# Kernel tuning notes

Measured on AMD Instinct MI355X. Metric: run time of the kernel, lower is better.

The kernel has to match this reference:

```python
import jax, jax.numpy as jnp
import numpy as np
from jax import lax

PRE_NMS_TOPN = 2000
POST_NMS_TOPN = 1000
NMS_THRESH = 0.7
MIN_BOX_SIZE = 4.0
BBOX_XFORM_CLIP = 4.135  # log(1000/16), standard clamp on dw/dh


def setup_inputs() -> dict:
    key = jax.random.key(0)
    k1, k2, k3, k4 = jax.random.split(key, 4)
    B, N = 8, 250000
    H, W = 800, 1333
    rpn_bbox_pred = jax.random.normal(k1, (B, N, 4), jnp.float32) * 0.5
    objectness = jax.random.normal(k2, (B, N), jnp.float32)
    # realistic anchors: centers inside image, sizes in [16, 256]
    ctr = jax.random.uniform(k3, (N, 2), jnp.float32) * jnp.array([W, H], jnp.float32)
    wh = jax.random.uniform(k4, (N, 2), jnp.float32) * 240.0 + 16.0
    anchors = jnp.concatenate([ctr - 0.5 * wh, ctr + 0.5 * wh], axis=-1)
    return {"rpn_bbox_pred": rpn_bbox_pred, "objectness": objectness,
            "anchors": anchors, "height": H, "width": W}


def _decode_clip(anchors, deltas, height, width):
    # anchors (1,N,4) broadcast against deltas (B,N,4); boxes are x1,y1,x2,y2
    aw = anchors[..., 2] - anchors[..., 0]
    ah = anchors[..., 3] - anchors[..., 1]
    ax = anchors[..., 0] + 0.5 * aw
    ay = anchors[..., 1] + 0.5 * ah
    dx, dy = deltas[..., 0], deltas[..., 1]
    dw = jnp.minimum(deltas[..., 2], BBOX_XFORM_CLIP)
    dh = jnp.minimum(deltas[..., 3], BBOX_XFORM_CLIP)
    px = dx * aw + ax
    py = dy * ah + ay
    pw = jnp.exp(dw) * aw
    ph = jnp.exp(dh) * ah
    x1 = jnp.clip(px - 0.5 * pw, 0.0, float(width))
    y1 = jnp.clip(py - 0.5 * ph, 0.0, float(height))
    x2 = jnp.clip(px + 0.5 * pw, 0.0, float(width))
    y2 = jnp.clip(py + 0.5 * ph, 0.0, float(height))
    return jnp.stack([x1, y1, x2, y2], axis=-1)


def _pairwise_iou(boxes):
    # boxes (K,4) -> iou (K,K)
    x1, y1, x2, y2 = boxes[:, 0], boxes[:, 1], boxes[:, 2], boxes[:, 3]
    area = (x2 - x1) * (y2 - y1)
    iw = jnp.maximum(jnp.minimum(x2[:, None], x2[None, :]) - jnp.maximum(x1[:, None], x1[None, :]), 0.0)
    ih = jnp.maximum(jnp.minimum(y2[:, None], y2[None, :]) - jnp.maximum(y1[:, None], y1[None, :]), 0.0)
    inter = iw * ih
    return inter / (area[:, None] + area[None, :] - inter + 1e-9)


def _nms_keep(boxes, valid):
    # sequential greedy NMS over score-sorted boxes (K,4); returns keep mask (K,)
    iou = lax.stop_gradient(_pairwise_iou(boxes))
    idxs = jnp.arange(PRE_NMS_TOPN)
    def body(i, keep):
        sup = (iou[i] > NMS_THRESH) & keep[i] & (idxs > i)
        return keep & (~sup)
    return lax.fori_loop(0, PRE_NMS_TOPN, body, valid)


def _per_image(boxes, scores):
    # boxes (N,4), scores (N,)
    ws = boxes[:, 2] - boxes[:, 0]
    hs = boxes[:, 3] - boxes[:, 1]
    size_ok = (ws >= MIN_BOX_SIZE) & (hs >= MIN_BOX_SIZE)
    masked = jnp.where(size_ok, scores, -jnp.inf)
    top_s, order = lax.top_k(masked, PRE_NMS_TOPN)   # descending sort + pre-NMS topN
    top_boxes = boxes[order]                          # (PRE,4)
    valid = top_s > -jnp.inf                          # boxes surviving size filter
    keep = _nms_keep(top_boxes, valid)
    # take first POST_NMS_TOPN kept boxes in score order (fixed-shape padding)
    sel = jnp.sort(jnp.where(keep, jnp.arange(PRE_NMS_TOPN), PRE_NMS_TOPN))[:POST_NMS_TOPN]
    out_valid = sel < PRE_NMS_TOPN
    sel_c = jnp.minimum(sel, PRE_NMS_TOPN - 1)
    out = jnp.where(out_valid[:, None], top_boxes[sel_c], 0.0)
    return out, out_valid


def reference(rpn_bbox_pred, objectness, anchors, height, width):
    proposals = _decode_clip(anchors[None], rpn_bbox_pred, height, width)  # (B,N,4)
    out, valid = jax.vmap(_per_image)(proposals, objectness)
    # padded equivalent of the ragged per-image list: (B,POST,4) boxes + (B,POST) validity
    return out, valid
```

## Files before the change

### kernel.cpp

```cpp
#include <hip/hip_runtime.h>
#include <hip/hip_bf16.h>

#define NBUCK 8192
#define P1B   32
#define CAP   4096
#define TOPN  2000
#define NP2   2048
#define OUTN  1000
#define NST   64
#define NSLOT 8
#define SLOTW 2048

typedef unsigned int u32x4 __attribute__((ext_vector_type(4)));
typedef __attribute__((address_space(1))) const unsigned GUP;
typedef __attribute__((address_space(3))) unsigned LUP;

__device__ __forceinline__ float4 decode_box(const float4 a, const float4 d, float W, float H) {
    float aw = a.z - a.x;
    float ah = a.w - a.y;
    float ax = a.x + 0.5f * aw;
    float ay = a.y + 0.5f * ah;
    float dw = fminf(d.z, 4.135f);
    float dh = fminf(d.w, 4.135f);
    float px = d.x * aw + ax;
    float py = d.y * ah + ay;
    float pw = expf(dw) * aw;
    float ph = expf(dh) * ah;
    float4 r;
    r.x = fminf(fmaxf(px - 0.5f * pw, 0.0f), W);
    r.y = fminf(fmaxf(py - 0.5f * ph, 0.0f), H);
    r.z = fminf(fmaxf(px + 0.5f * pw, 0.0f), W);
    r.w = fminf(fmaxf(py + 0.5f * ph, 0.0f), H);
    return r;
}

__device__ __forceinline__ unsigned score_key(const float4 a, const float4 d, float W, float H, float s) {
    float4 b = decode_box(a, d, W, H);
    bool ok = ((b.z - b.x) >= 4.0f) && ((b.w - b.y) >= 4.0f);
    float ms = ok ? s : -INFINITY;
    unsigned u = __float_as_uint(ms);
    return (u & 0x80000000u) ? ~u : (u | 0x80000000u);
}

__global__ void k_zero(u32x4* __restrict__ hist) {
    hist[blockIdx.x * 256 + threadIdx.x] = (u32x4){0u, 0u, 0u, 0u};
}

__global__ void __launch_bounds__(1024) k_pass1(const float* __restrict__ pred,
        const float* __restrict__ obj, const float* __restrict__ anch,
        const int* __restrict__ Hp, const int* __restrict__ Wp,
        unsigned* __restrict__ keys, unsigned* __restrict__ hist,
        unsigned* __restrict__ cnt, unsigned* __restrict__ remInit, int N) {
    __shared__ unsigned h[2 * NBUCK];
    int t = threadIdx.x;
    int b = blockIdx.y, g = blockIdx.x;
    if (g == 0 && t < 64) { if (t == 0) cnt[b * 64] = 0; remInit[b * 64 + t] = 0; }
    for (int i = t; i < 2 * NBUCK; i += 1024) h[i] = 0;
    __syncthreads();
    int chunk = (N + P1B - 1) / P1B;
    int base = g * chunk;
    int end = base + chunk; if (end > N) end = N;
    float W = (float)*Wp, H = (float)*Hp;
    unsigned cp = (t & 1) ? NBUCK : 0;
    for (int n = base + t; n < end; n += 1024) {
        float4 a = ((const float4*)anch)[n];
        float4 d = ((const float4*)pred)[(size_t)b * N + n];
        float s = obj[(size_t)b * N + n];
        unsigned key = score_key(a, d, W, H, s);
        keys[(size_t)b * N + n] = key;
        atomicAdd(&h[cp + (key >> 19)], 1u);
    }
    __syncthreads();
    for (int i = t; i < NBUCK; i += 1024) {
        unsigned v = h[i] + h[NBUCK + i];
        if (v) atomicAdd(&hist[b * NBUCK + i], v);
    }
}

__global__ void k_scan(const unsigned* __restrict__ hist, unsigned* __restrict__ Lb) {
    __shared__ unsigned h[NBUCK];
    __shared__ unsigned csum[256];
    __shared__ unsigned suf[256];
    __shared__ int tcS;
    __shared__ unsigned beforeS;
    int b = blockIdx.x, t = threadIdx.x;
    const unsigned* src = hist + (size_t)b * NBUCK;
    for (int i = t * 4; i < NBUCK; i += 1024) {
        uint4 v = *(const uint4*)(src + i);
        h[i] = v.x; h[i + 1] = v.y; h[i + 2] = v.z; h[i + 3] = v.w;
    }
    if (t == 0) tcS = -1;
    __syncthreads();
    unsigned s = 0;
    for (int j = 0; j < 32; j++) s += h[t * 32 + j];
    csum[t] = s; suf[t] = s;
    __syncthreads();
    for (int d = 1; d < 256; d <<= 1) {
        unsigned v = (t + d < 256) ? suf[t + d] : 0;
        __syncthreads();
        suf[t] += v;
        __syncthreads();
    }
    if (suf[t] >= (unsigned)TOPN && (t == 255 || suf[t + 1] < (unsigned)TOPN)) {
        tcS = t; beforeS = (t == 255) ? 0u : suf[t + 1];
    }
    __syncthreads();
    if (t == 0) {
        unsigned L = 0;
        int tc = tcS;
        if (tc >= 0) {
            unsigned r = beforeS;
            for (int bkt = tc * 32 + 31;; bkt--) {
                r += h[bkt];
                if (r >= (unsigned)TOPN || bkt == tc * 32) { L = (unsigned)bkt; break; }
            }
        }
        Lb[b] = L;
    }
}

__global__ void k_collect(const unsigned* __restrict__ keys, const unsigned* __restrict__ Lb,
                          unsigned* __restrict__ count, unsigned long long* __restrict__ cand,
                          int N) {
    __shared__ unsigned lk[1024], ln[1024];
    __shared__ unsigned lcnt, lbase;
    int b = blockIdx.y, t = threadIdx.x;
    if (t == 0) lcnt = 0;
    __syncthreads();
    unsigned L = Lb[b];
    const unsigned* kb = keys + (size_t)b * N;
    int e = blockIdx.x * 256 + t;
    int n0 = e * 4;
    if (n0 + 3 < N) {
        uint4 kv = ((const uint4*)kb)[e];
        if ((kv.x >> 19) >= L) { unsigned p = atomicAdd(&lcnt, 1u); lk[p] = kv.x; ln[p] = n0; }
        if ((kv.y >> 19) >= L) { unsigned p = atomicAdd(&lcnt, 1u); lk[p] = kv.y; ln[p] = n0 + 1; }
        if ((kv.z >> 19) >= L) { unsigned p = atomicAdd(&lcnt, 1u); lk[p] = kv.z; ln[p] = n0 + 2; }
        if ((kv.w >> 19) >= L) { unsigned p = atomicAdd(&lcnt, 1u); lk[p] = kv.w; ln[p] = n0 + 3; }
    } else {
        for (int j = 0; j < 4; j++) {
            int n = n0 + j;
            if (n < N) {
                unsigned k = kb[n];
                if ((k >> 19) >= L) { unsigned p = atomicAdd(&lcnt, 1u); lk[p] = k; ln[p] = n; }
            }
        }
    }
    __syncthreads();
    if (t == 0) lbase = atomicAdd(&count[b * 64], lcnt);
    __syncthreads();
    unsigned c = lcnt, bs = lbase;
    for (unsigned i = t; i < c; i += 256) {
        unsigned pos = bs + i;
        if (pos < CAP) cand[(size_t)b * CAP + pos] =
            ((unsigned long long)lk[i] << 32) | (unsigned)(~ln[i]);
    }
}

#define REGX(e, p, d, lo)  ((lo) == (d) ? ((e) >= (p) ? (e) : (p)) : ((e) >= (p) ? (p) : (e)))

__global__ void __launch_bounds__(256) k_sort1(unsigned long long* __restrict__ cand,
        const unsigned* __restrict__ count) {
    __shared__ unsigned long long s[512];
    int b = blockIdx.x >> 3, g = blockIdx.x & 7;
    int t = threadIdx.x;
    unsigned cnt = count[b * 64]; if (cnt > CAP) cnt = CAP;
    unsigned long long* cb = cand + (size_t)b * CAP + g * 512;
    if ((unsigned)(g * 512) >= cnt) {
        cb[t] = 0ULL; cb[t + 256] = 0ULL;
        return;
    }
    int g0 = g * 512 + t, g1 = g * 512 + t + 256;
    unsigned long long e0 = (g0 < (int)cnt) ? cb[t] : 0ULL;
    unsigned long long e1 = (g1 < (int)cnt) ? cb[t + 256] : 0ULL;

    #pragma unroll
    for (int k = 2; k <= 64; k <<= 1) {
        bool d0 = ((g0 & k) == 0);
        bool d1 = ((g1 & k) == 0);
        #pragma unroll
        for (int j = k >> 1; j >= 1; j >>= 1) {
            bool lo = ((t & j) == 0);
            unsigned long long p0 = __shfl_xor(e0, j, 64);
            unsigned long long p1 = __shfl_xor(e1, j, 64);
            e0 = REGX(e0, p0, d0, lo);
            e1 = REGX(e1, p1, d1, lo);
        }
    }
    for (int k = 128; k <= 512; k <<= 1) {
        s[t] = e0; s[t + 256] = e1;
        __syncthreads();
        for (int j = k >> 1; j >= 64; j >>= 1) {
            int i = ((t & ~(j - 1)) << 1) | (t & (j - 1));
            int l = i + j;
            bool desc = (((g * 512 + i) & k) == 0);
            unsigned long long x = s[i], y = s[l];
            if (desc ? (x < y) : (x > y)) { s[i] = y; s[l] = x; }
            __syncthreads();
        }
        e0 = s[t]; e1 = s[t + 256];
        bool d0 = ((g0 & k) == 0);
        bool d1 = ((g1 & k) == 0);
        #pragma unroll
        for (int j = 32; j >= 1; j >>= 1) {
            bool lo = ((t & j) == 0);
            unsigned long long p0 = __shfl_xor(e0, j, 64);
            unsigned long long p1 = __shfl_xor(e1, j, 64);
            e0 = REGX(e0, p0, d0, lo);
            e1 = REGX(e1, p1, d1, lo);
        }
    }
    cb[t] = e0; cb[t + 256] = e1;
}

__global__ void __launch_bounds__(1024) k_sort2(const unsigned long long* __restrict__ cand,
        const unsigned* __restrict__ count,
        const float* __restrict__ pred, const float* __restrict__ anch,
        const int* __restrict__ Hp, const int* __restrict__ Wp,
        float4* __restrict__ topbox, unsigned* __restrict__ remInit, int N) {
    __shared__ unsigned long long s[CAP];
    int b = blockIdx.x, t = threadIdx.x;
    const unsigned long long* cb = cand + (size_t)b * CAP;
    unsigned cnt = count[b * 64]; if (cnt > CAP) cnt = CAP;
    unsigned long long e0, e1;
    if (cnt <= 2048) {
        e0 = cb[t]; e1 = cb[t + 1024];
        for (int k = 1024; k <= 2048; k <<= 1) {
            s[t] = e0; s[t + 1024] = e1;
            __syncthreads();
            for (int j = k >> 1; j >= 64; j >>= 1) {
                int i = ((t & ~(j - 1)) << 1) | (t & (j - 1));
                int l = i + j;
                bool desc = ((i & k) == 0);
                unsigned long long x = s[i], y = s[l];
                if (desc ? (x < y) : (x > y)) { s[i] = y; s[l] = x; }
                __syncthreads();
            }
            e0 = s[t]; e1 = s[t + 1024];
            bool d0 = ((t & k) == 0);
            bool d1 = (((t + 1024) & k) == 0);
            #pragma unroll
            for (int j = 32; j >= 1; j >>= 1) {
                bool lo = ((t & j) == 0);
                unsigned long long p0 = __shfl_xor(e0, j, 64);
                unsigned long long p1 = __shfl_xor(e1, j, 64);
                e0 = REGX(e0, p0, d0, lo);
                e1 = REGX(e1, p1, d1, lo);
            }
        }
    } else {
        unsigned long long f0 = cb[t], f1 = cb[t + 1024], f2 = cb[t + 2048], f3 = cb[t + 3072];
        for (int k = 1024; k <= 4096; k <<= 1) {
            s[t] = f0; s[t + 1024] = f1; s[t + 2048] = f2; s[t + 3072] = f3;
            __syncthreads();
            for (int j = k >> 1; j >= 64; j >>= 1) {
                #pragma unroll
                for (int cc = 0; cc < 2; cc++) {
                    int c = t + cc * 1024;
                    int i = ((c & ~(j - 1)) << 1) | (c & (j - 1));
                    int l = i + j;
                    bool desc = ((i & k) == 0);
                    unsigned long long x = s[i], y = s[l];
                    if (desc ? (x < y) : (x > y)) { s[i] = y; s[l] = x; }
                }
                __syncthreads();
            }
            f0 = s[t]; f1 = s[t + 1024]; f2 = s[t + 2048]; f3 = s[t + 3072];
            bool d0 = ((t & k) == 0);
            bool d1 = (((t + 1024) & k) == 0);
            bool d2 = (((t + 2048) & k) == 0);
            bool d3 = (((t + 3072) & k) == 0);
            #pragma unroll
            for (int j = 32; j >= 1; j >>= 1) {
                bool lo = ((t & j) == 0);
                unsigned long long p0 = __shfl_xor(f0, j, 64);
                unsigned long long p1 = __shfl_xor(f1, j, 64);
                unsigned long long p2 = __shfl_xor(f2, j, 64);
                unsigned long long p3 = __shfl_xor(f3, j, 64);
                f0 = REGX(f0, p0, d0, lo);
                f1 = REGX(f1, p1, d1, lo);
                f2 = REGX(f2, p2, d2, lo);
                f3 = REGX(f3, p3, d3, lo);
            }
        }
        e0 = f0; e1 = f1;
    }
    float W = (float)*Wp, H = (float)*Hp;
    #pragma unroll
    for (int m = 0; m < 2; m++) {
        unsigned long long v = m ? e1 : e0;
        int r = t + m * 1024;
        unsigned key = (unsigned)(v >> 32);
        bool valid = key > 0x007FFFFFu;
        float4 outb = {0.f, 0.f, 0.f, 0.f};
        if (valid) {
            unsigned idx = ~((unsigned)v);
            float4 a = ((const float4*)anch)[idx];
            float4 d = ((const float4*)pred)[(size_t)b * N + idx];
            outb = decode_box(a, d, W, H);
        }
        topbox[(size_t)b * NP2 + r] = outb;
        if (r < TOPN && !valid) atomicOr(&remInit[b * 64 + (r >> 5)], 1u << (r & 31));
    }
}

__global__ void __launch_bounds__(256) k_mask(const float4* __restrict__ topbox,
                                              unsigned* __restrict__ maskT) {
    const double MID = 23488103.0 / 33554432.0;
    __shared__ float4 bx[NP2];
    __shared__ float ar[NP2];
    int b = blockIdx.y, cp = blockIdx.x;
    int t = threadIdx.x;
    int j0 = cp * 32;
    for (int i = j0 + t; i < NP2; i += 256) {
        float4 v = topbox[(size_t)b * NP2 + i];
        bx[i] = v;
        ar[i] = (v.z - v.x) * (v.w - v.y);
    }
    __syncthreads();
    int r = t & 31;
    int wg = t >> 5;
    #pragma unroll
    for (int half = 0; half < 2; half++) {
        int c = half ? (63 - cp) : cp;
        int i = c * 32 + r;
        float4 bi = bx[i];
        float areai = ar[i];
        unsigned* outc = maskT + ((size_t)(b * NST + c)) * SLOTW;
        for (int w = wg; w < c; w += 8) outc[w * 32 + r] = 0u;
        for (int w = c + wg; w < 64; w += 8) {
            unsigned bits = 0;
            int jbase = w * 32;
            #pragma unroll
            for (int jj = 0; jj < 32; jj++) {
                int j = jbase + jj;
                float4 bj = bx[j];
                float iw = fmaxf(fminf(bi.z, bj.z) - fmaxf(bi.x, bj.x), 0.0f);
                float ih = fmaxf(fminf(bi.w, bj.w) - fmaxf(bi.y, bj.y), 0.0f);
                float inter = iw * ih;
                float denom = areai + ar[j] - inter + 1e-9f;
                if ((double)inter >= MID * (double)denom) bits |= (1u << jj);
            }
            if (w == c) bits &= ~((2u << r) - 1u);
            outc[w * 32 + r] = bits;
        }
    }
}

__global__ void __launch_bounds__(512) k_nms(const unsigned* __restrict__ maskT,
        const unsigned* __restrict__ remInit, const float4* __restrict__ topbox,
        float* __restrict__ out, int B) {
    __shared__ __align__(16) unsigned smbuf[NSLOT * SLOTW];
    __shared__ int ready[NST];
    __shared__ int consumed;
    __shared__ int stop;
    int b = blockIdx.x;
    int t = threadIdx.x;
    const unsigned* m = maskT + (size_t)b * NST * SLOTW;

    float4* ob = (float4*)out + (size_t)b * OUTN;
    for (int i = t; i < OUTN; i += 512) ob[i] = make_float4(0.f, 0.f, 0.f, 0.f);
    float* vout = out + (size_t)B * (OUTN * 4) + (size_t)b * OUTN;
    for (int i = t; i < OUTN; i += 512) vout[i] = 0.0f;

    if (t < NST) ready[t] = 0;
    if (t == 0) { consumed = 0; stop = 0; }
    __syncthreads();

    unsigned removed = 0xFFFFFFFFu;

    if (t >= 64) {
        int w = t >> 6;
        int lam = t & 63;
        int base = ((lam >> 3) << 5) + ((((lam & 7) ^ ((lam >> 3) & 7))) << 2);
        #pragma unroll 1
        for (int s = w - 1; s < NST; s += 7) {
            if (__hip_atomic_load(&stop, __ATOMIC_RELAXED, __HIP_MEMORY_SCOPE_WORKGROUP)) break;
            while (__hip_atomic_load(&consumed, __ATOMIC_ACQUIRE,
                   __HIP_MEMORY_SCOPE_WORKGROUP) < s - (NSLOT - 1))
                __builtin_amdgcn_s_sleep(2);
            const unsigned* gs = m + (size_t)s * SLOTW + base;
            unsigned* sl = smbuf + (s & (NSLOT - 1)) * SLOTW;
            #pragma unroll
            for (int i = 0; i < 8; i++)
                __builtin_amdgcn_global_load_lds((GUP*)(gs + i * 256),
                                                 (LUP*)(sl + i * 256), 16, 0, 0);
            asm volatile("s_waitcnt vmcnt(0)" ::: "memory");
            if (lam == 0) __hip_atomic_store(&ready[s], 1, __ATOMIC_RELEASE,
                                             __HIP_MEMORY_SCOPE_WORKGROUP);
        }
    } else {
        removed = remInit[b * 64 + t];
        if (t == 62) removed |= 0xFFFF0000u;
        if (t == 63) removed = 0xFFFFFFFFu;
        int e = t & 7;
        int keptRun = 0;
        #pragma unroll 1
        for (int s = 0; s < NST; s++) {
            while (!__hip_atomic_load(&ready[s], __ATOMIC_ACQUIRE,
                   __HIP_MEMORY_SCOPE_WORKGROUP))
                __builtin_amdgcn_s_sleep(2);
            const u32x4* sq = (const u32x4*)(smbuf + (s & (NSLOT - 1)) * SLOTW) + t * 8;
            unsigned R[32];
            #pragma unroll
            for (int k = 0; k < 8; k++) *(u32x4*)&R[k << 2] = sq[k ^ e];
            __builtin_amdgcn_sched_group_barrier(0x100, 8, 0);
            unsigned alive = ~__builtin_amdgcn_readlane(removed, s);
            unsigned Is[32];
            #pragma unroll
            for (int q = 0; q < 32; q++) Is[q] = __builtin_amdgcn_readlane(R[q], s);
            #pragma unroll
            for (int q = 0; q < 32; q++) alive &= ~(((alive >> q) & 1u) ? Is[q] : 0u);
            unsigned a0 = 0, a1 = 0, a2 = 0, a3 = 0;
            #pragma unroll
            for (int q = 0; q < 32; q += 4) {
                a0 |= ((alive >> q) & 1u)       ? R[q]     : 0u;
                a1 |= ((alive >> (q + 1)) & 1u) ? R[q + 1] : 0u;
                a2 |= ((alive >> (q + 2)) & 1u) ? R[q + 2] : 0u;
                a3 |= ((alive >> (q + 3)) & 1u) ? R[q + 3] : 0u;
            }
            removed |= (a0 | a1) | (a2 | a3);
            keptRun += __popc(~__builtin_amdgcn_readlane(removed, s));
            if (keptRun >= OUTN) {
                if (t == 0) {
                    __hip_atomic_store(&stop, 1, __ATOMIC_RELAXED, __HIP_MEMORY_SCOPE_WORKGROUP);
                    __hip_atomic_store(&consumed, NST, __ATOMIC_RELEASE, __HIP_MEMORY_SCOPE_WORKGROUP);
                }
                break;
            }
            if (t == 0) __hip_atomic_store(&consumed, s + 1, __ATOMIC_RELEASE,
                                           __HIP_MEMORY_SCOPE_WORKGROUP);
        }
        unsigned keep = ~removed;
        int cnt = __popc(keep);
        int ex = cnt;
        for (int off = 1; off < 64; off <<= 1) {
            int v = __shfl_up(ex, off, 64);
            if (t >= off) ex += v;
        }
        ex -= cnt;
        int pos = ex;
        for (int j = 0; j < 32; j++) {
            if ((keep >> j) & 1u) {
                if (pos < OUTN) {
                    float4 bxv = topbox[(size_t)b * NP2 + t * 32 + j];
                    ob[pos] = bxv;
                    vout[pos] = 1.0f;
                }
                pos++;
            }
        }
    }
}

extern "C" void kernel_launch(void* const* d_in, const int* in_sizes, int n_in,
                              void* d_out, int out_size, void* d_ws, size_t ws_size,
                              hipStream_t stream) {
    const float* pred = (const float*)d_in[0];
    const float* obj  = (const float*)d_in[1];
    const float* anch = (const float*)d_in[2];
    const int* Hp = (const int*)d_in[3];
    const int* Wp = (const int*)d_in[4];
    int N = in_sizes[2] / 4;
    int B = in_sizes[1] / N;

    char* ws = (char*)d_ws;
    size_t off = 0;
    auto take = [&](size_t bytes) { void* p = ws + off; off = (off + bytes + 255) & ~(size_t)255; return p; };

    size_t regA_bytes = (size_t)B * N * 4;
    size_t mask_bytes = (size_t)B * NST * SLOTW * 4;
    char* regA = (char*)take(regA_bytes > mask_bytes ? regA_bytes : mask_bytes);
    unsigned* keys  = (unsigned*)regA;
    unsigned* maskT = (unsigned*)regA;
    unsigned* hist           = (unsigned*)take((size_t)B * NBUCK * 4);
    unsigned long long* cand = (unsigned long long*)take((size_t)B * CAP * 8);
    float4* topbox           = (float4*)take((size_t)B * NP2 * 16);
    unsigned* cnt            = (unsigned*)take((size_t)B * 64 * 4);
    unsigned* Lb             = (unsigned*)take((size_t)B * 64 * 4);
    unsigned* remInit        = (unsigned*)take((size_t)B * 64 * 4);

    k_zero   <<<(B * NBUCK) / 1024, 256, 0, stream>>>((u32x4*)hist);
    k_pass1  <<<dim3(P1B, B), 1024, 0, stream>>>(pred, obj, anch, Hp, Wp, keys, hist, cnt, remInit, N);
    k_scan   <<<B, 256, 0, stream>>>(hist, Lb);
    k_collect<<<dim3((N + 1023) / 1024, B), 256, 0, stream>>>(keys, Lb, cnt, cand, N);
    k_sort1  <<<B * 8, 256, 0, stream>>>(cand, cnt);
    k_sort2  <<<B, 1024, 0, stream>>>(cand, cnt, pred, anch, Hp, Wp, topbox, remInit, N);
    k_mask   <<<dim3(32, B), 256, 0, stream>>>(topbox, maskT);
    k_nms    <<<B, 512, 0, stream>>>(maskT, remInit, topbox, (float*)d_out, B);
}
```

Baseline: 118.2 us.

## Fuse histogram scan into pass1 via last-block election; coarsen collect blocks

After: 131.5 us. 11.2% more time.

```diff
diff --git a/kernel.cpp b/kernel.cpp
--- a/kernel.cpp
+++ b/kernel.cpp
@@ -42,16 +42,19 @@
     return (u & 0x80000000u) ? ~u : (u | 0x80000000u);
 }
 
-__global__ void k_zero(u32x4* __restrict__ hist) {
-    hist[blockIdx.x * 256 + threadIdx.x] = (u32x4){0u, 0u, 0u, 0u};
+__global__ void k_zero(unsigned* __restrict__ p, int nq) {
+    int i = blockIdx.x * 256 + threadIdx.x;
+    if (i < nq) ((u32x4*)p)[i] = (u32x4){0u, 0u, 0u, 0u};
 }
 
 __global__ void __launch_bounds__(1024) k_pass1(const float* __restrict__ pred,
         const float* __restrict__ obj, const float* __restrict__ anch,
         const int* __restrict__ Hp, const int* __restrict__ Wp,
         unsigned* __restrict__ keys, unsigned* __restrict__ hist,
+        unsigned* __restrict__ done, unsigned* __restrict__ Lb,
         unsigned* __restrict__ cnt, unsigned* __restrict__ remInit, int N) {
     __shared__ unsigned h[2 * NBUCK];
+    __shared__ int lastFlag;
     int t = threadIdx.x;
     int b = blockIdx.y, g = blockIdx.x;
     if (g == 0 && t < 64) { if (t == 0) cnt[b * 64] = 0; remInit[b * 64 + t] = 0; }
@@ -75,41 +78,45 @@
         unsigned v = h[i] + h[NBUCK + i];
         if (v) atomicAdd(&hist[b * NBUCK + i], v);
     }
-}
-
-__global__ void k_scan(const unsigned* __restrict__ hist, unsigned* __restrict__ Lb) {
-    __shared__ unsigned h[NBUCK];
-    __shared__ unsigned csum[256];
-    __shared__ unsigned suf[256];
-    __shared__ int tcS;
-    __shared__ unsigned beforeS;
-    int b = blockIdx.x, t = threadIdx.x;
-    const unsigned* src = hist + (size_t)b * NBUCK;
-    for (int i = t * 4; i < NBUCK; i += 1024) {
-        uint4 v = *(const uint4*)(src + i);
-        h[i] = v.x; h[i + 1] = v.y; h[i + 2] = v.z; h[i + 3] = v.w;
-    }
-    if (t == 0) tcS = -1;
-    __syncthreads();
-    unsigned s = 0;
-    for (int j = 0; j < 32; j++) s += h[t * 32 + j];
-    csum[t] = s; suf[t] = s;
+    if (t == 0) {
+        __threadfence();
+        unsigned dcnt = __hip_atomic_fetch_add(&done[b], 1u, __ATOMIC_ACQ_REL,
+                                               __HIP_MEMORY_SCOPE_AGENT);
+        lastFlag = (dcnt == P1B - 1);
+    }
+    __syncthreads();
+    if (!lastFlag) return;
+    __threadfence();
+    unsigned* csum = h + NBUCK;
+    unsigned* suf  = h + NBUCK + 256;
+    int*      tcS  = (int*)(h + NBUCK + 512);
+    unsigned* befS = h + NBUCK + 513;
+    for (int i = t; i < NBUCK; i += 1024)
+        h[i] = __hip_atomic_load(&hist[b * NBUCK + i], __ATOMIC_RELAXED,
+                                 __HIP_MEMORY_SCOPE_AGENT);
+    if (t == 0) *tcS = -1;
+    __syncthreads();
+    if (t < 256) {
+        unsigned s = 0;
+        for (int j = 0; j < 32; j++) s += h[t * 32 + j];
+        csum[t] = s; suf[t] = s;
+    }
     __syncthreads();
     for (int d = 1; d < 256; d <<= 1) {
-        unsigned v = (t + d < 256) ? suf[t + d] : 0;
-        __syncthreads();
-        suf[t] += v;
-        __syncthreads();
-    }
-    if (suf[t] >= (unsigned)TOPN && (t == 255 || suf[t + 1] < (unsigned)TOPN)) {
-        tcS = t; beforeS = (t == 255) ? 0u : suf[t + 1];
+        unsigned v = (t < 256 && t + d < 256) ? suf[t + d] : 0;
+        __syncthreads();
+        if (t < 256) suf[t] += v;
+        __syncthreads();
+    }
+    if (t < 256 && suf[t] >= (unsigned)TOPN && (t == 255 || suf[t + 1] < (unsigned)TOPN)) {
+        *tcS = t; *befS = (t == 255) ? 0u : suf[t + 1];
     }
     __syncthreads();
     if (t == 0) {
         unsigned L = 0;
-        int tc = tcS;
+        int tc = *tcS;
         if (tc >= 0) {
-            unsigned r = beforeS;
+            unsigned r = *befS;
             for (int bkt = tc * 32 + 31;; bkt--) {
                 r += h[bkt];
                 if (r >= (unsigned)TOPN || bkt == tc * 32) { L = (unsigned)bkt; break; }
@@ -125,35 +132,39 @@
     __shared__ unsigned lk[1024], ln[1024];
     __shared__ unsigned lcnt, lbase;
     int b = blockIdx.y, t = threadIdx.x;
-    if (t == 0) lcnt = 0;
-    __syncthreads();
     unsigned L = Lb[b];
     const unsigned* kb = keys + (size_t)b * N;
-    int e = blockIdx.x * 256 + t;
-    int n0 = e * 4;
-    if (n0 + 3 < N) {
-        uint4 kv = ((const uint4*)kb)[e];
-        if ((kv.x >> 19) >= L) { unsigned p = atomicAdd(&lcnt, 1u); lk[p] = kv.x; ln[p] = n0; }
-        if ((kv.y >> 19) >= L) { unsigned p = atomicAdd(&lcnt, 1u); lk[p] = kv.y; ln[p] = n0 + 1; }
-        if ((kv.z >> 19) >= L) { unsigned p = atomicAdd(&lcnt, 1u); lk[p] = kv.z; ln[p] = n0 + 2; }
-        if ((kv.w >> 19) >= L) { unsigned p = atomicAdd(&lcnt, 1u); lk[p] = kv.w; ln[p] = n0 + 3; }
-    } else {
-        for (int j = 0; j < 4; j++) {
-            int n = n0 + j;
-            if (n < N) {
-                unsigned k = kb[n];
-                if ((k >> 19) >= L) { unsigned p = atomicAdd(&lcnt, 1u); lk[p] = k; ln[p] = n; }
-            }
-        }
-    }
-    __syncthreads();
-    if (t == 0) lbase = atomicAdd(&count[b * 64], lcnt);
-    __syncthreads();
-    unsigned c = lcnt, bs = lbase;
-    for (unsigned i = t; i < c; i += 256) {
-        unsigned pos = bs + i;
-        if (pos < CAP) cand[(size_t)b * CAP + pos] =
-            ((unsigned long long)lk[i] << 32) | (unsigned)(~ln[i]);
+    int base4 = blockIdx.x * 1024;
+    for (int it = 0; it < 4; it++) {
+        if (t == 0) lcnt = 0;
+        __syncthreads();
+        int e = base4 + it * 256 + t;
+        int n0 = e * 4;
+        if (n0 + 3 < N) {
+            uint4 kv = ((const uint4*)kb)[e];
+            if ((kv.x >> 19) >= L) { unsigned p = atomicAdd(&lcnt, 1u); lk[p] = kv.x; ln[p] = n0; }
+            if ((kv.y >> 19) >= L) { unsigned p = atomicAdd(&lcnt, 1u); lk[p] = kv.y; ln[p] = n0 + 1; }
+            if ((kv.z >> 19) >= L) { unsigned p = atomicAdd(&lcnt, 1u); lk[p] = kv.z; ln[p] = n0 + 2; }
+            if ((kv.w >> 19) >= L) { unsigned p = atomicAdd(&lcnt, 1u); lk[p] = kv.w; ln[p] = n0 + 3; }
+        } else {
+            for (int j = 0; j < 4; j++) {
+                int n = n0 + j;
+                if (n < N) {
+                    unsigned k = kb[n];
+                    if ((k >> 19) >= L) { unsigned p = atomicAdd(&lcnt, 1u); lk[p] = k; ln[p] = n; }
+                }
+            }
+        }
+        __syncthreads();
+        if (t == 0 && lcnt) lbase = atomicAdd(&count[b * 64], lcnt);
+        __syncthreads();
+        unsigned c = lcnt, bs = lbase;
+        for (unsigned i = t; i < c; i += 256) {
+            unsigned pos = bs + i;
+            if (pos < CAP) cand[(size_t)b * CAP + pos] =
+                ((unsigned long long)lk[i] << 32) | (unsigned)(~ln[i]);
+        }
+        __syncthreads();
     }
 }
 
@@ -473,17 +484,19 @@
     char* regA = (char*)take(regA_bytes > mask_bytes ? regA_bytes : mask_bytes);
     unsigned* keys  = (unsigned*)regA;
     unsigned* maskT = (unsigned*)regA;
-    unsigned* hist           = (unsigned*)take((size_t)B * NBUCK * 4);
+    int zwords = B * NBUCK + 64;
+    unsigned* hist           = (unsigned*)take((size_t)zwords * 4);
+    unsigned* done           = hist + B * NBUCK;
     unsigned long long* cand = (unsigned long long*)take((size_t)B * CAP * 8);
     float4* topbox           = (float4*)take((size_t)B * NP2 * 16);
     unsigned* cnt            = (unsigned*)take((size_t)B * 64 * 4);
     unsigned* Lb             = (unsigned*)take((size_t)B * 64 * 4);
     unsigned* remInit        = (unsigned*)take((size_t)B * 64 * 4);
 
-    k_zero   <<<(B * NBUCK) / 1024, 256, 0, stream>>>((u32x4*)hist);
-    k_pass1  <<<dim3(P1B, B), 1024, 0, stream>>>(pred, obj, anch, Hp, Wp, keys, hist, cnt, remInit, N);
-    k_scan   <<<B, 256, 0, stream>>>(hist, Lb);
-    k_collect<<<dim3((N + 1023) / 1024, B), 256, 0, stream>>>(keys, Lb, cnt, cand, N);
+    int nq = (zwords + 3) / 4;
+    k_zero   <<<(nq + 255) / 256, 256, 0, stream>>>(hist, nq);
+    k_pass1  <<<dim3(P1B, B), 1024, 0, stream>>>(pred, obj, anch, Hp, Wp, keys, hist, done, Lb, cnt, remInit, N);
+    k_collect<<<dim3((N + 4095) / 4096, B), 256, 0, stream>>>(keys, Lb, cnt, cand, N);
     k_sort1  <<<B * 8, 256, 0, stream>>>(cand, cnt);
     k_sort2  <<<B, 1024, 0, stream>>>(cand, cnt, pred, anch, Hp, Wp, topbox, remInit, N);
     k_mask   <<<dim3(32, B), 256, 0, stream>>>(topbox, maskT);
```

## Replace global histogram atomics with per-block 16-bit histograms reduced in scan

Applied to the files above, without the earlier changes.

After: 122.0 us. +3.2%, slower.

```diff
diff --git a/kernel.cpp b/kernel.cpp
--- a/kernel.cpp
+++ b/kernel.cpp
@@ -2,7 +2,7 @@
 #include <hip/hip_bf16.h>
 
 #define NBUCK 8192
-#define P1B   32
+#define P1B   64
 #define CAP   4096
 #define TOPN  2000
 #define NP2   2048
@@ -42,74 +42,83 @@
     return (u & 0x80000000u) ? ~u : (u | 0x80000000u);
 }
 
-__global__ void k_zero(u32x4* __restrict__ hist) {
-    hist[blockIdx.x * 256 + threadIdx.x] = (u32x4){0u, 0u, 0u, 0u};
-}
-
 __global__ void __launch_bounds__(1024) k_pass1(const float* __restrict__ pred,
         const float* __restrict__ obj, const float* __restrict__ anch,
         const int* __restrict__ Hp, const int* __restrict__ Wp,
-        unsigned* __restrict__ keys, unsigned* __restrict__ hist,
+        unsigned* __restrict__ keys, unsigned short* __restrict__ bhist,
         unsigned* __restrict__ cnt, unsigned* __restrict__ remInit, int N) {
-    __shared__ unsigned h[2 * NBUCK];
+    __shared__ unsigned h[NBUCK];
     int t = threadIdx.x;
     int b = blockIdx.y, g = blockIdx.x;
     if (g == 0 && t < 64) { if (t == 0) cnt[b * 64] = 0; remInit[b * 64 + t] = 0; }
-    for (int i = t; i < 2 * NBUCK; i += 1024) h[i] = 0;
+    for (int i = t; i < NBUCK; i += 1024) h[i] = 0;
     __syncthreads();
     int chunk = (N + P1B - 1) / P1B;
     int base = g * chunk;
     int end = base + chunk; if (end > N) end = N;
     float W = (float)*Wp, H = (float)*Hp;
-    unsigned cp = (t & 1) ? NBUCK : 0;
     for (int n = base + t; n < end; n += 1024) {
         float4 a = ((const float4*)anch)[n];
         float4 d = ((const float4*)pred)[(size_t)b * N + n];
         float s = obj[(size_t)b * N + n];
         unsigned key = score_key(a, d, W, H, s);
         keys[(size_t)b * N + n] = key;
-        atomicAdd(&h[cp + (key >> 19)], 1u);
-    }
-    __syncthreads();
-    for (int i = t; i < NBUCK; i += 1024) {
-        unsigned v = h[i] + h[NBUCK + i];
-        if (v) atomicAdd(&hist[b * NBUCK + i], v);
-    }
-}
-
-__global__ void k_scan(const unsigned* __restrict__ hist, unsigned* __restrict__ Lb) {
+        atomicAdd(&h[key >> 19], 1u);
+    }
+    __syncthreads();
+    unsigned short* bh = bhist + ((size_t)(b * P1B + g)) * NBUCK;
+    int i0 = t * 8;
+    uint4 pk;
+    pk.x = (h[i0 + 0] & 0xFFFFu) | (h[i0 + 1] << 16);
+    pk.y = (h[i0 + 2] & 0xFFFFu) | (h[i0 + 3] << 16);
+    pk.z = (h[i0 + 4] & 0xFFFFu) | (h[i0 + 5] << 16);
+    pk.w = (h[i0 + 6] & 0xFFFFu) | (h[i0 + 7] << 16);
+    *(uint4*)(bh + i0) = pk;
+}
+
+__global__ void __launch_bounds__(1024) k_scan(const unsigned short* __restrict__ bhist,
+                                               unsigned* __restrict__ Lb) {
     __shared__ unsigned h[NBUCK];
     __shared__ unsigned csum[256];
     __shared__ unsigned suf[256];
     __shared__ int tcS;
-    __shared__ unsigned beforeS;
+    __shared__ unsigned befS;
     int b = blockIdx.x, t = threadIdx.x;
-    const unsigned* src = hist + (size_t)b * NBUCK;
-    for (int i = t * 4; i < NBUCK; i += 1024) {
-        uint4 v = *(const uint4*)(src + i);
-        h[i] = v.x; h[i + 1] = v.y; h[i + 2] = v.z; h[i + 3] = v.w;
-    }
+    const unsigned short* src = bhist + (size_t)b * P1B * NBUCK;
+    int i0 = t * 8;
+    unsigned acc[8] = {0, 0, 0, 0, 0, 0, 0, 0};
+    for (int g = 0; g < P1B; g++) {
+        uint4 v = *(const uint4*)(src + (size_t)g * NBUCK + i0);
+        acc[0] += v.x & 0xFFFFu; acc[1] += v.x >> 16;
+        acc[2] += v.y & 0xFFFFu; acc[3] += v.y >> 16;
+        acc[4] += v.z & 0xFFFFu; acc[5] += v.z >> 16;
+        acc[6] += v.w & 0xFFFFu; acc[7] += v.w >> 16;
+    }
+    #pragma unroll
+    for (int k = 0; k < 8; k++) h[i0 + k] = acc[k];
     if (t == 0) tcS = -1;
     __syncthreads();
-    unsigned s = 0;
-    for (int j = 0; j < 32; j++) s += h[t * 32 + j];
-    csum[t] = s; suf[t] = s;
+    if (t < 256) {
+        unsigned s = 0;
+        for (int j = 0; j < 32; j++) s += h[t * 32 + j];
+        csum[t] = s; suf[t] = s;
+    }
     __syncthreads();
     for (int d = 1; d < 256; d <<= 1) {
-        unsigned v = (t + d < 256) ? suf[t + d] : 0;
+        unsigned v = (t < 256 && t + d < 256) ? suf[t + d] : 0;
         __syncthreads();
-        suf[t] += v;
+        if (t < 256) suf[t] += v;
         __syncthreads();
     }
-    if (suf[t] >= (unsigned)TOPN && (t == 255 || suf[t + 1] < (unsigned)TOPN)) {
-        tcS = t; beforeS = (t == 255) ? 0u : suf[t + 1];
+    if (t < 256 && suf[t] >= (unsigned)TOPN && (t == 255 || suf[t + 1] < (unsigned)TOPN)) {
+        tcS = t; befS = (t == 255) ? 0u : suf[t + 1];
     }
     __syncthreads();
     if (t == 0) {
         unsigned L = 0;
         int tc = tcS;
         if (tc >= 0) {
-            unsigned r = beforeS;
+            unsigned r = befS;
             for (int bkt = tc * 32 + 31;; bkt--) {
                 r += h[bkt];
                 if (r >= (unsigned)TOPN || bkt == tc * 32) { L = (unsigned)bkt; break; }
@@ -473,16 +482,15 @@
     char* regA = (char*)take(regA_bytes > mask_bytes ? regA_bytes : mask_bytes);
     unsigned* keys  = (unsigned*)regA;
     unsigned* maskT = (unsigned*)regA;
-    unsigned* hist           = (unsigned*)take((size_t)B * NBUCK * 4);
+    unsigned short* bhist    = (unsigned short*)take((size_t)B * P1B * NBUCK * 2);
     unsigned long long* cand = (unsigned long long*)take((size_t)B * CAP * 8);
     float4* topbox           = (float4*)take((size_t)B * NP2 * 16);
     unsigned* cnt            = (unsigned*)take((size_t)B * 64 * 4);
     unsigned* Lb             = (unsigned*)take((size_t)B * 64 * 4);
     unsigned* remInit        = (unsigned*)take((size_t)B * 64 * 4);
 
-    k_zero   <<<(B * NBUCK) / 1024, 256, 0, stream>>>((u32x4*)hist);
-    k_pass1  <<<dim3(P1B, B), 1024, 0, stream>>>(pred, obj, anch, Hp, Wp, keys, hist, cnt, remInit, N);
-    k_scan   <<<B, 256, 0, stream>>>(hist, Lb);
+    k_pass1  <<<dim3(P1B, B), 1024, 0, stream>>>(pred, obj, anch, Hp, Wp, keys, bhist, cnt, remInit, N);
+    k_scan   <<<B, 1024, 0, stream>>>(bhist, Lb);
     k_collect<<<dim3((N + 1023) / 1024, B), 256, 0, stream>>>(keys, Lb, cnt, cand, N);
     k_sort1  <<<B * 8, 256, 0, stream>>>(cand, cnt);
     k_sort2  <<<B, 1024, 0, stream>>>(cand, cnt, pred, anch, Hp, Wp, topbox, remInit, N);
```
